# Performance work log

Hardware: AMD Instinct MI355X
Metric: run time of the kernel (lower is better)

## Reference

```python
import jax, jax.numpy as jnp
import numpy as np

NUM_HEADS = 16

def setup_inputs() -> dict:
    key = jax.random.key(0)
    k1, k2, k3 = jax.random.split(key, 3)
    B, N, C = 4, 4096, 1024
    x = jax.random.normal(k1, (B, N, C), dtype=jnp.float32)
    # xavier-uniform-ish scaled init for the dense kernels
    w_qkv = jax.random.normal(k2, (C, 3 * C), dtype=jnp.float32) * (2.0 / (C + 3 * C)) ** 0.5
    w_proj = jax.random.normal(k3, (C, C), dtype=jnp.float32) * (1.0 / C) ** 0.5
    b_proj = jnp.zeros((C,), dtype=jnp.float32)
    return {"x": x, "w_qkv": w_qkv, "w_proj": w_proj, "b_proj": b_proj}

def reference(x, w_qkv, w_proj, b_proj):
    B, N, C = x.shape
    H = NUM_HEADS
    D = C // H
    # qkv projection: (B, N, 3C) -> (3, B, H, N, D)
    qkv = (x @ w_qkv).reshape(B, N, 3, H, D).transpose(2, 0, 3, 1, 4)
    q, k, v = qkv[0], qkv[1], qkv[2]
    # feature map: elu + 1 (positive features)
    q = jax.nn.elu(q) + 1.0
    k = jax.nn.elu(k) + 1.0
    # kv outer-product accumulation: (B, H, D, D)
    kv = jnp.einsum('bhnd,bhne->bhde', k, v)
    numerator = jnp.einsum('bhnd,bhde->bhne', q, kv)        # (B, H, N, D)
    sum_k = k.sum(axis=-2)                                   # (B, H, D)
    denominator = jnp.einsum('bhnd,bhd->bhn', q, sum_k)[..., None]  # (B, H, N, 1)
    y = numerator / denominator                              # (B, H, N, D)
    y = y.transpose(0, 2, 1, 3).reshape(B, N, C)             # merge heads
    out = y @ w_proj + b_proj
    return out
```

## Files before the change

kernel.cpp:

```cpp
#include <hip/hip_runtime.h>

typedef __bf16 bf16x8 __attribute__((ext_vector_type(8)));
typedef float f32x4 __attribute__((ext_vector_type(4)));

typedef const unsigned int __attribute__((address_space(1)))* gas_p;
typedef unsigned int __attribute__((address_space(3)))* las_p;

__device__ __forceinline__ void gload_lds16(const void* g, void* l) {
  __builtin_amdgcn_global_load_lds((gas_p)g, (las_p)l, 16, 0, 0);
}

__device__ __forceinline__ unsigned short f2bf(float f) {
  union { float f; unsigned int u; } x; x.f = f;
  unsigned int r = x.u + 0x7fffu + ((x.u >> 16) & 1u);
  return (unsigned short)(r >> 16);
}
__device__ __forceinline__ float elu1(float x) {
  return x > 0.f ? x + 1.f : __expf(x);
}
__device__ __forceinline__ f32x4 mfma16(bf16x8 a, bf16x8 b, f32x4 c) {
  return __builtin_amdgcn_mfma_f32_16x16x32_bf16(a, b, c, 0, 0, 0);
}

#define BAR() __builtin_amdgcn_s_barrier()
#define VMW4() asm volatile("s_waitcnt vmcnt(4)" ::: "memory")


__global__ __launch_bounds__(256) void k_cvt_x(const float* __restrict__ x,
                                               unsigned short* __restrict__ xb, int n) {
  int i = (blockIdx.x * 256 + threadIdx.x) * 4;
  const int stride = gridDim.x * 256 * 4;
  for (; i < n; i += stride) {
    float4 v = *(const float4*)(x + i);
    union { unsigned short u[4]; uint2 q; } pk;
    pk.u[0] = f2bf(v.x); pk.u[1] = f2bf(v.y); pk.u[2] = f2bf(v.z); pk.u[3] = f2bf(v.w);
    *(uint2*)(xb + i) = pk.q;
  }
}

__global__ __launch_bounds__(256) void k_cvt_t(const float* __restrict__ w,
                                               unsigned short* __restrict__ wT,
                                               int R, int Cc) {
  __shared__ float t[32][33];
  const int j0 = blockIdx.x * 32, i0 = blockIdx.y * 32;
  const int tx = threadIdx.x & 31, ty = threadIdx.x >> 5;
#pragma unroll
  for (int k = 0; k < 4; ++k)
    t[ty + 8 * k][tx] = w[(size_t)(i0 + ty + 8 * k) * Cc + j0 + tx];
  __syncthreads();
#pragma unroll
  for (int k = 0; k < 4; ++k)
    wT[(size_t)(j0 + ty + 8 * k) * R + i0 + tx] = f2bf(t[tx][ty + 8 * k]);
}


template <int EPI>
__global__ __launch_bounds__(512, 2) void k_gemm256(
    const unsigned short* __restrict__ A, const unsigned short* __restrict__ BT, int NBX,
    unsigned short* __restrict__ qb, unsigned short* __restrict__ kT,
    unsigned short* __restrict__ vT, const float* __restrict__ bias,
    float* __restrict__ out) {
  extern __shared__ unsigned short lds[];
  unsigned short* Asb = lds;
  unsigned short* Bsb = lds + 32768;

  const int tid = threadIdx.x, lane = tid & 63, wave = tid >> 6;
  const int wm = wave >> 2, wn = wave & 3;
  int bid = blockIdx.x;
  { const int cpx = (int)gridDim.x >> 3; bid = (bid & 7) * cpx + (bid >> 3); }
  const int bx = bid % NBX, by = bid / NBX;
  const size_t bm0 = (size_t)by << 8, bn0 = (size_t)bx << 8;

  const int srow = (wave << 4) + (lane >> 2);
  const int scol = (lane & 3) << 3;
  const unsigned short* Ag0 = A + (bm0 + srow) * 1024 + scol;
  const unsigned short* Bg0 = BT + (bn0 + srow) * 1024 + scol;
  unsigned short* Al0 = Asb + (wave << 9);
  unsigned short* Bl0 = Bsb + (wave << 9);

#define STAGE_A(OBH, KT)                                          \
  do {                                                            \
    const unsigned short* g_ = Ag0 + ((KT) << 6) + (OBH_K);       \
    unsigned short* l_ = Al0 + (OBH);                             \
    gload_lds16(g_, l_);                                          \
    gload_lds16(g_ + 128 * 1024, l_ + 4096);                      \
  } while (0)
#define STAGE_B(OBH, KT)                                          \
  do {                                                            \
    const unsigned short* g_ = Bg0 + ((KT) << 6) + (OBH_K);       \
    unsigned short* l_ = Bl0 + (OBH);                             \
    gload_lds16(g_, l_);                                          \
    gload_lds16(g_ + 128 * 1024, l_ + 4096);                      \
  } while (0)

  const int q8 = (lane >> 4) << 3;
  const int ar_base = (wm << 7) + (lane & 15);
  const int br_base = (wn << 6) + (lane & 15);

  f32x4 acc[8][4] = {};

  {
#define OBH_K 0
    STAGE_A(0, 0);
    STAGE_B(0, 0);
#undef OBH_K
#define OBH_K 32
    STAGE_A(8192, 0);
    STAGE_B(8192, 0);
#undef OBH_K
  }
  VMW4();
  BAR();

  for (int kt = 0; kt < 16; ++kt) {
    const int ob = (kt & 1) << 14;
    const int obn = ob ^ 16384;
    const int ktn = (kt < 15) ? kt + 1 : 15;
    bf16x8 af[4], bfr[4];

#pragma unroll
    for (int mi = 0; mi < 4; ++mi)
      af[mi] = *(const bf16x8*)&Asb[ob + ((ar_base + mi * 16) << 5) + q8];
#pragma unroll
    for (int n = 0; n < 4; ++n)
      bfr[n] = *(const bf16x8*)&Bsb[ob + ((br_base + n * 16) << 5) + q8];
#define OBH_K 0
    STAGE_A(obn, ktn);
#undef OBH_K
    BAR();
    __builtin_amdgcn_s_setprio(1);
#pragma unroll
    for (int mi = 0; mi < 4; ++mi)
#pragma unroll
      for (int n = 0; n < 4; ++n) acc[mi][n] = mfma16(af[mi], bfr[n], acc[mi][n]);
    __builtin_amdgcn_s_setprio(0);
    BAR();

#pragma unroll
    for (int mi = 0; mi < 4; ++mi)
      af[mi] = *(const bf16x8*)&Asb[ob + ((ar_base + 64 + mi * 16) << 5) + q8];
#define OBH_K 0
    STAGE_B(obn, ktn);
#undef OBH_K
    BAR();
    __builtin_amdgcn_s_setprio(1);
#pragma unroll
    for (int mi = 0; mi < 4; ++mi)
#pragma unroll
      for (int n = 0; n < 4; ++n) acc[4 + mi][n] = mfma16(af[mi], bfr[n], acc[4 + mi][n]);
    __builtin_amdgcn_s_setprio(0);
    VMW4();
    BAR();

#pragma unroll
    for (int mi = 0; mi < 4; ++mi)
      af[mi] = *(const bf16x8*)&Asb[ob + 8192 + ((ar_base + mi * 16) << 5) + q8];
#pragma unroll
    for (int n = 0; n < 4; ++n)
      bfr[n] = *(const bf16x8*)&Bsb[ob + 8192 + ((br_base + n * 16) << 5) + q8];
#define OBH_K 32
    STAGE_A(obn + 8192, ktn);
#undef OBH_K
    BAR();
    __builtin_amdgcn_s_setprio(1);
#pragma unroll
    for (int mi = 0; mi < 4; ++mi)
#pragma unroll
      for (int n = 0; n < 4; ++n) acc[mi][n] = mfma16(af[mi], bfr[n], acc[mi][n]);
    __builtin_amdgcn_s_setprio(0);
    BAR();

#pragma unroll
    for (int mi = 0; mi < 4; ++mi)
      af[mi] = *(const bf16x8*)&Asb[ob + 8192 + ((ar_base + 64 + mi * 16) << 5) + q8];
#define OBH_K 32
    STAGE_B(obn + 8192, ktn);
#undef OBH_K
    BAR();
    __builtin_amdgcn_s_setprio(1);
#pragma unroll
    for (int mi = 0; mi < 4; ++mi)
#pragma unroll
      for (int n = 0; n < 4; ++n) acc[4 + mi][n] = mfma16(af[mi], bfr[n], acc[4 + mi][n]);
    __builtin_amdgcn_s_setprio(0);
    VMW4();
    BAR();
  }

  const int rbase = (int)bm0 + (wm << 7) + ((lane >> 4) << 2);
  const int cbase = (int)bn0 + (wn << 6) + (lane & 15);
  if constexpr (EPI == 0) {
    const int reg3 = (int)(bn0 >> 10);
#pragma unroll
    for (int m = 0; m < 8; ++m) {
      const int rb = rbase + m * 16;
#pragma unroll
      for (int n = 0; n < 4; ++n) {
        const int col = cbase + n * 16;
        if (reg3 == 0) {
#pragma unroll
          for (int i = 0; i < 4; ++i)
            qb[(size_t)(rb + i) * 1024 + col] = f2bf(elu1(acc[m][n][i]));
        } else {
          const int jc = col & 1023, h = jc >> 6, d = jc & 63;
          const int b_ = rb >> 12, n_ = rb & 4095;
          union { unsigned short u[4]; uint2 q; } pk;
          if (reg3 == 1) {
#pragma unroll
            for (int i = 0; i < 4; ++i) pk.u[i] = f2bf(elu1(acc[m][n][i]));
          } else {
#pragma unroll
            for (int i = 0; i < 4; ++i) pk.u[i] = f2bf(acc[m][n][i]);
          }
          unsigned short* dst = (reg3 == 1) ? kT : vT;
          *(uint2*)(dst + ((size_t)((b_ * 16 + h) * 64 + d) * 4096 + n_)) = pk.q;
        }
      }
    }
  } else {
#pragma unroll
    for (int n = 0; n < 4; ++n) {
      const int col = cbase + n * 16;
      const float bc = bias[col];
#pragma unroll
      for (int m = 0; m < 8; ++m) {
        const int rb = rbase + m * 16;
#pragma unroll
        for (int i = 0; i < 4; ++i)
          out[(size_t)(rb + i) * 1024 + col] = acc[m][n][i] + bc;
      }
    }
  }
#undef STAGE_A
#undef STAGE_B
}


__device__ __forceinline__ float bfsum2(unsigned int w) {
  union { unsigned int u; float f; } a, b;
  a.u = w << 16; b.u = w & 0xffff0000u;
  return a.f + b.f;
}

__global__ __launch_bounds__(256) void k_sumk(const unsigned short* __restrict__ kT,
                                              float* __restrict__ sumk) {
  const int row = (blockIdx.x << 2) + (threadIdx.x >> 6);
  const int lane = threadIdx.x & 63;
  const unsigned short* p = kT + (size_t)row * 4096;
  float s = 0.f;
#pragma unroll
  for (int i = 0; i < 8; ++i) {
    uint4 v = *(const uint4*)(p + (i * 64 + lane) * 8);
    s += bfsum2(v.x) + bfsum2(v.y) + bfsum2(v.z) + bfsum2(v.w);
  }
#pragma unroll
  for (int off = 32; off > 0; off >>= 1) s += __shfl_down(s, off);
  if (lane == 0) sumk[row] = s;
}


__global__ __launch_bounds__(256) void k_kvpart(const unsigned short* __restrict__ kT,
                                                const unsigned short* __restrict__ vT,
                                                float* __restrict__ kvp) {
  __shared__ unsigned short Ks[64 * 64];
  __shared__ unsigned short Vs[64 * 64];
  const int blk = blockIdx.x;
  const int bh = blk >> 3, ch = blk & 7;
  const int tid = threadIdx.x, lane = tid & 63, wave = tid >> 6;
  const unsigned short* kb = kT + (size_t)bh * 64 * 4096;
  const unsigned short* vb = vT + (size_t)bh * 64 * 4096;
  const int n0 = ch * 512;
  const int lrow = lane >> 3, lcol = (lane & 7) << 3;
  f32x4 acc[4] = {};

  for (int ks = 0; ks < 512; ks += 64) {
    __syncthreads();
#pragma unroll
    for (int i = 0; i < 2; ++i) {
      const int c = i * 4 + wave;
      gload_lds16(kb + (size_t)(c * 8 + lrow) * 4096 + n0 + ks + lcol, &Ks[c * 512]);
      gload_lds16(vb + (size_t)(c * 8 + lrow) * 4096 + n0 + ks + lcol, &Vs[c * 512]);
    }
    __syncthreads();
    const int ko = (lane >> 4) << 3;
    const int ar = wave * 16 + (lane & 15);
#pragma unroll
    for (int kk = 0; kk < 2; ++kk) {
      bf16x8 a = *(const bf16x8*)&Ks[ar * 64 + ko + kk * 32];
#pragma unroll
      for (int n = 0; n < 4; ++n) {
        bf16x8 bv = *(const bf16x8*)&Vs[(n * 16 + (lane & 15)) * 64 + ko + kk * 32];
        acc[n] = mfma16(a, bv, acc[n]);
      }
    }
  }
  float* dst = kvp + (size_t)blk * 64 * 64;
  const int d0 = wave * 16 + ((lane >> 4) << 2);
#pragma unroll
  for (int n = 0; n < 4; ++n)
#pragma unroll
    for (int i = 0; i < 4; ++i)
      dst[(d0 + i) * 64 + n * 16 + (lane & 15)] = acc[n][i];
}


__global__ __launch_bounds__(256) void k_kvred(const float* __restrict__ kvp,
                                               const float* __restrict__ sumk,
                                               unsigned short* __restrict__ kvsk) {
  const int bh = blockIdx.x, tid = threadIdx.x;
  const float* src = kvp + (size_t)bh * 8 * 4096;
  unsigned short* dst = kvsk + (size_t)bh * 80 * 64;
#pragma unroll
  for (int it = 0; it < 16; ++it) {
    const int idx = tid + it * 256;
    const int e = idx >> 6, d = idx & 63;
    float s = 0.f;
#pragma unroll
    for (int c = 0; c < 8; ++c) s += src[c * 4096 + d * 64 + e];
    dst[idx] = f2bf(s);
  }
#pragma unroll
  for (int it = 0; it < 4; ++it) {
    const int idx = tid + it * 256;
    const int e2 = idx >> 6, d = idx & 63;
    float v = (e2 == 0) ? sumk[bh * 64 + d] : 0.f;
    dst[64 * 64 + idx] = f2bf(v);
  }
}


__global__ __launch_bounds__(256) void k_numer(const unsigned short* __restrict__ qb,
                                               const unsigned short* __restrict__ kvsk,
                                               unsigned short* __restrict__ yb) {
  __shared__ unsigned short Bs[80 * 64];
  const int bh = blockIdx.y;
  const int b = bh >> 4, h = bh & 15;
  const int n0 = blockIdx.x << 7;
  const int tid = threadIdx.x, lane = tid & 63, wave = tid >> 6;
  {
    const uint4* src = (const uint4*)(kvsk + (size_t)bh * 80 * 64);
    uint4* dst = (uint4*)Bs;
    for (int i = tid; i < 640; i += 256) dst[i] = src[i];
  }
  __syncthreads();

  const int ko = (lane >> 4) << 3;
  f32x4 acc[2][5] = {};
  const unsigned short* qrow =
      qb + (size_t)(b * 4096 + n0 + wave * 32 + (lane & 15)) * 1024 + h * 64;
#pragma unroll
  for (int kk = 0; kk < 2; ++kk) {
    bf16x8 a[2], bb[5];
#pragma unroll
    for (int m = 0; m < 2; ++m)
      a[m] = *(const bf16x8*)(qrow + (size_t)m * 16 * 1024 + ko + kk * 32);
#pragma unroll
    for (int n = 0; n < 5; ++n)
      bb[n] = *(const bf16x8*)&Bs[(n * 16 + (lane & 15)) * 64 + ko + kk * 32];
#pragma unroll
    for (int m = 0; m < 2; ++m)
#pragma unroll
      for (int n = 0; n < 5; ++n)
        acc[m][n] = mfma16(a[m], bb[n], acc[m][n]);
  }

  const int rbase = b * 4096 + n0 + wave * 32 + ((lane >> 4) << 2);
#pragma unroll
  for (int m = 0; m < 2; ++m) {
    f32x4 inv;
#pragma unroll
    for (int i = 0; i < 4; ++i) {
      float den = __shfl(acc[m][4][i], lane & 48);
      inv[i] = __builtin_amdgcn_rcpf(den);
    }
#pragma unroll
    for (int n = 0; n < 4; ++n) {
      const int col = h * 64 + n * 16 + (lane & 15);
#pragma unroll
      for (int i = 0; i < 4; ++i)
        yb[(size_t)(rbase + m * 16 + i) * 1024 + col] = f2bf(acc[m][n][i] * inv[i]);
    }
  }
}


extern "C" void kernel_launch(void* const* d_in, const int* in_sizes, int n_in,
                              void* d_out, int out_size, void* d_ws, size_t ws_size,
                              hipStream_t stream) {
  const float* x = (const float*)d_in[0];
  const float* w_qkv = (const float*)d_in[1];
  const float* w_proj = (const float*)d_in[2];
  const float* b_proj = (const float*)d_in[3];
  float* out = (float*)d_out;
  char* ws = (char*)d_ws;

  unsigned short* xb = (unsigned short*)(ws);
  unsigned short* wqkvT = (unsigned short*)(ws + 33554432);
  unsigned short* wprojT = (unsigned short*)(ws + 39845888);
  unsigned short* qb = (unsigned short*)(ws + 41943040);
  unsigned short* kT = (unsigned short*)(ws + 75497472);
  unsigned short* vT = (unsigned short*)(ws + 109051904);
  float* kvp = (float*)(ws + 142606336);
  float* sumk = (float*)(ws + 150994944);
  unsigned short* kvsk = (unsigned short*)(ws + 151011328);
  unsigned short* yb = xb;

  k_cvt_x<<<2048, 256, 0, stream>>>(x, xb, 4 * 4096 * 1024);
  k_cvt_t<<<dim3(96, 32), 256, 0, stream>>>(w_qkv, wqkvT, 1024, 3072);
  k_cvt_t<<<dim3(32, 32), 256, 0, stream>>>(w_proj, wprojT, 1024, 1024);
  k_gemm256<0><<<768, 512, 131072, stream>>>(xb, wqkvT, 12, qb, kT, vT, nullptr, nullptr);
  k_sumk<<<1024, 256, 0, stream>>>(kT, sumk);
  k_kvpart<<<512, 256, 0, stream>>>(kT, vT, kvp);
  k_kvred<<<64, 256, 0, stream>>>(kvp, sumk, kvsk);
  k_numer<<<dim3(32, 64), 256, 0, stream>>>(qb, kvsk, yb);
  k_gemm256<1><<<256, 512, 131072, stream>>>(yb, wprojT, 4, nullptr, nullptr, nullptr,
                                             b_proj, out);
}
```

Baseline: 236.0 us.

## Fuse key-sum into kv MFMA kernel and XOR-swizzle LDS tiles

Drops the separate k_sumk pass. Per-chunk key sums are now computed inside k_kvpart with an extra MFMA against a ones fragment, and k_kvred reduces those partials. The LDS tiles in the big GEMM, kvpart and numer kernels are XOR-swizzled: global source columns are permuted at load time and read offsets are adjusted to match, which is meant to cut LDS bank conflicts. This removes one kernel launch and a re-read of kT, at the cost of an extra MFMA per step and reusing the wqkvT workspace (dead after the QKV GEMM) for the partial sums.

After: 222.8 us. 1.06x faster.

```diff
diff --git a/kernel.cpp b/kernel.cpp
--- a/kernel.cpp
+++ b/kernel.cpp
@@ -72,9 +72,9 @@
   const size_t bm0 = (size_t)by << 8, bn0 = (size_t)bx << 8;
 
   const int srow = (wave << 4) + (lane >> 2);
-  const int scol = (lane & 3) << 3;
-  const unsigned short* Ag0 = A + (bm0 + srow) * 1024 + scol;
-  const unsigned short* Bg0 = BT + (bn0 + srow) * 1024 + scol;
+  const int gscol = ((lane & 3) << 3) ^ (((srow >> 1) & 3) << 3);
+  const unsigned short* Ag0 = A + (bm0 + srow) * 1024 + gscol;
+  const unsigned short* Bg0 = BT + (bn0 + srow) * 1024 + gscol;
   unsigned short* Al0 = Asb + (wave << 9);
   unsigned short* Bl0 = Bsb + (wave << 9);
 
@@ -93,7 +93,7 @@
     gload_lds16(g_ + 128 * 1024, l_ + 4096);                      \
   } while (0)
 
-  const int q8 = (lane >> 4) << 3;
+  const int q8 = (((lane >> 4) << 3)) ^ (((lane >> 1) & 3) << 3);
   const int ar_base = (wm << 7) + (lane & 15);
   const int br_base = (wn << 6) + (lane & 15);
 
@@ -236,32 +236,10 @@
 }
 
 
-__device__ __forceinline__ float bfsum2(unsigned int w) {
-  union { unsigned int u; float f; } a, b;
-  a.u = w << 16; b.u = w & 0xffff0000u;
-  return a.f + b.f;
-}
-
-__global__ __launch_bounds__(256) void k_sumk(const unsigned short* __restrict__ kT,
-                                              float* __restrict__ sumk) {
-  const int row = (blockIdx.x << 2) + (threadIdx.x >> 6);
-  const int lane = threadIdx.x & 63;
-  const unsigned short* p = kT + (size_t)row * 4096;
-  float s = 0.f;
-#pragma unroll
-  for (int i = 0; i < 8; ++i) {
-    uint4 v = *(const uint4*)(p + (i * 64 + lane) * 8);
-    s += bfsum2(v.x) + bfsum2(v.y) + bfsum2(v.z) + bfsum2(v.w);
-  }
-#pragma unroll
-  for (int off = 32; off > 0; off >>= 1) s += __shfl_down(s, off);
-  if (lane == 0) sumk[row] = s;
-}
-
-
 __global__ __launch_bounds__(256) void k_kvpart(const unsigned short* __restrict__ kT,
                                                 const unsigned short* __restrict__ vT,
-                                                float* __restrict__ kvp) {
+                                                float* __restrict__ kvp,
+                                                float* __restrict__ sumkp) {
   __shared__ unsigned short Ks[64 * 64];
   __shared__ unsigned short Vs[64 * 64];
   const int blk = blockIdx.x;
@@ -270,28 +248,43 @@
   const unsigned short* kb = kT + (size_t)bh * 64 * 4096;
   const unsigned short* vb = vT + (size_t)bh * 64 * 4096;
   const int n0 = ch * 512;
-  const int lrow = lane >> 3, lcol = (lane & 7) << 3;
-  f32x4 acc[4] = {};
+  const int lrow = lane >> 3;
+  const int lcolz = (((lane & 7) ^ (lane >> 3)) << 3);
+  f32x4 acc[5] = {};
+
+  bf16x8 ones_frag;
+  {
+    unsigned short o = ((lane & 15) == 0) ? (unsigned short)0x3F80 : (unsigned short)0;
+    union { unsigned short u[8]; bf16x8 v; } c;
+#pragma unroll
+    for (int i = 0; i < 8; ++i) c.u[i] = o;
+    ones_frag = c.v;
+  }
+
+  const int rxor = (lane & 7) << 3;
+  const int col0 = (((lane >> 4) << 3)) ^ rxor;
+  const int col1 = ((32 + ((lane >> 4) << 3))) ^ rxor;
 
   for (int ks = 0; ks < 512; ks += 64) {
     __syncthreads();
 #pragma unroll
     for (int i = 0; i < 2; ++i) {
       const int c = i * 4 + wave;
-      gload_lds16(kb + (size_t)(c * 8 + lrow) * 4096 + n0 + ks + lcol, &Ks[c * 512]);
-      gload_lds16(vb + (size_t)(c * 8 + lrow) * 4096 + n0 + ks + lcol, &Vs[c * 512]);
+      gload_lds16(kb + (size_t)(c * 8 + lrow) * 4096 + n0 + ks + lcolz, &Ks[c * 512]);
+      gload_lds16(vb + (size_t)(c * 8 + lrow) * 4096 + n0 + ks + lcolz, &Vs[c * 512]);
     }
     __syncthreads();
-    const int ko = (lane >> 4) << 3;
     const int ar = wave * 16 + (lane & 15);
 #pragma unroll
     for (int kk = 0; kk < 2; ++kk) {
-      bf16x8 a = *(const bf16x8*)&Ks[ar * 64 + ko + kk * 32];
+      const int co = kk ? col1 : col0;
+      bf16x8 a = *(const bf16x8*)&Ks[ar * 64 + co];
 #pragma unroll
       for (int n = 0; n < 4; ++n) {
-        bf16x8 bv = *(const bf16x8*)&Vs[(n * 16 + (lane & 15)) * 64 + ko + kk * 32];
+        bf16x8 bv = *(const bf16x8*)&Vs[(n * 16 + (lane & 15)) * 64 + co];
         acc[n] = mfma16(a, bv, acc[n]);
       }
+      acc[4] = mfma16(a, ones_frag, acc[4]);
     }
   }
   float* dst = kvp + (size_t)blk * 64 * 64;
@@ -301,11 +294,15 @@
 #pragma unroll
     for (int i = 0; i < 4; ++i)
       dst[(d0 + i) * 64 + n * 16 + (lane & 15)] = acc[n][i];
+  if ((lane & 15) == 0) {
+#pragma unroll
+    for (int i = 0; i < 4; ++i) sumkp[(size_t)blk * 64 + d0 + i] = acc[4][i];
+  }
 }
 
 
 __global__ __launch_bounds__(256) void k_kvred(const float* __restrict__ kvp,
-                                               const float* __restrict__ sumk,
+                                               const float* __restrict__ sumkp,
                                                unsigned short* __restrict__ kvsk) {
   const int bh = blockIdx.x, tid = threadIdx.x;
   const float* src = kvp + (size_t)bh * 8 * 4096;
@@ -323,7 +320,11 @@
   for (int it = 0; it < 4; ++it) {
     const int idx = tid + it * 256;
     const int e2 = idx >> 6, d = idx & 63;
-    float v = (e2 == 0) ? sumk[bh * 64 + d] : 0.f;
+    float v = 0.f;
+    if (e2 == 0) {
+#pragma unroll
+      for (int c = 0; c < 8; ++c) v += sumkp[(size_t)(bh * 8 + c) * 64 + d];
+    }
     dst[64 * 64 + idx] = f2bf(v);
   }
 }
@@ -340,11 +341,12 @@
   {
     const uint4* src = (const uint4*)(kvsk + (size_t)bh * 80 * 64);
     uint4* dst = (uint4*)Bs;
-    for (int i = tid; i < 640; i += 256) dst[i] = src[i];
+    for (int i = tid; i < 640; i += 256) dst[i ^ ((i >> 3) & 7)] = src[i];
   }
   __syncthreads();
 
   const int ko = (lane >> 4) << 3;
+  const int rx = (lane & 7) << 3;
   f32x4 acc[2][5] = {};
   const unsigned short* qrow =
       qb + (size_t)(b * 4096 + n0 + wave * 32 + (lane & 15)) * 1024 + h * 64;
@@ -356,7 +358,7 @@
       a[m] = *(const bf16x8*)(qrow + (size_t)m * 16 * 1024 + ko + kk * 32);
 #pragma unroll
     for (int n = 0; n < 5; ++n)
-      bb[n] = *(const bf16x8*)&Bs[(n * 16 + (lane & 15)) * 64 + ko + kk * 32];
+      bb[n] = *(const bf16x8*)&Bs[(n * 16 + (lane & 15)) * 64 + ((ko + kk * 32) ^ rx)];
 #pragma unroll
     for (int m = 0; m < 2; ++m)
 #pragma unroll
@@ -401,17 +403,16 @@
   unsigned short* kT = (unsigned short*)(ws + 75497472);
   unsigned short* vT = (unsigned short*)(ws + 109051904);
   float* kvp = (float*)(ws + 142606336);
-  float* sumk = (float*)(ws + 150994944);
   unsigned short* kvsk = (unsigned short*)(ws + 151011328);
   unsigned short* yb = xb;
+  float* sumkp = (float*)wqkvT;
 
   k_cvt_x<<<2048, 256, 0, stream>>>(x, xb, 4 * 4096 * 1024);
   k_cvt_t<<<dim3(96, 32), 256, 0, stream>>>(w_qkv, wqkvT, 1024, 3072);
   k_cvt_t<<<dim3(32, 32), 256, 0, stream>>>(w_proj, wprojT, 1024, 1024);
   k_gemm256<0><<<768, 512, 131072, stream>>>(xb, wqkvT, 12, qb, kT, vT, nullptr, nullptr);
-  k_sumk<<<1024, 256, 0, stream>>>(kT, sumk);
-  k_kvpart<<<512, 256, 0, stream>>>(kT, vT, kvp);
-  k_kvred<<<64, 256, 0, stream>>>(kvp, sumk, kvsk);
+  k_kvpart<<<512, 256, 0, stream>>>(kT, vT, kvp, sumkp);
+  k_kvred<<<64, 256, 0, stream>>>(kvp, sumkp, kvsk);
   k_numer<<<dim3(32, 64), 256, 0, stream>>>(qb, kvsk, yb);
   k_gemm256<1><<<256, 512, 131072, stream>>>(yb, wprojT, 4, nullptr, nullptr, nullptr,
                                              b_proj, out);
```
